# Performance work log

Measured on AMD Instinct MI355X. Metric: run time of the kernel, lower is better.

## Reference

```python
import jax, jax.numpy as jnp
import numpy as np

D_MODEL = 1024
NUM_HEADS = 16
HEAD_DIM = D_MODEL // NUM_HEADS
SCALE = 1.0 / np.sqrt(HEAD_DIM).astype(np.float32)


def setup_inputs() -> dict:
    key = jax.random.key(0)
    k1, k2, k3, k4 = jax.random.split(key, 4)
    B, L = 1, 4096
    s = 0.02
    x = jax.random.normal(k1, (B, L, D_MODEL), dtype=jnp.float32)
    W_qkv = jax.random.normal(k2, (D_MODEL, 3 * D_MODEL), dtype=jnp.float32) * s
    W_o = jax.random.normal(k3, (D_MODEL, D_MODEL), dtype=jnp.float32) * s
    b_o = jax.random.normal(k4, (D_MODEL,), dtype=jnp.float32) * s
    return {"x": x, "W_qkv": W_qkv, "W_o": W_o, "b_o": b_o}


def reference(x, W_qkv, W_o, b_o):
    B, L, D = x.shape
    H, Hd = NUM_HEADS, HEAD_DIM
    qkv = x @ W_qkv                          # [B, L, 3D]
    qkv = qkv.reshape(B, L, 3, H, Hd)
    q = jnp.transpose(qkv[:, :, 0], (0, 2, 1, 3))  # [B, H, L, Hd]
    k = jnp.transpose(qkv[:, :, 1], (0, 2, 1, 3))
    v = jnp.transpose(qkv[:, :, 2], (0, 2, 1, 3))
    scores = jnp.einsum("bhqd,bhkd->bhqk", q, k) * SCALE  # [B, H, L, L]
    attn = jax.nn.softmax(scores, axis=-1)
    out = jnp.einsum("bhqk,bhkd->bhqd", attn, v)          # [B, H, L, Hd]
    out = jnp.transpose(out, (0, 2, 1, 3)).reshape(B, L, D)
    return out @ W_o + b_o
```

## Files before the change

kernel.cpp:

```cpp
#include <hip/hip_runtime.h>
#include <stdint.h>


#define L_SEQ 4096
#define DM 1024
#define NHEAD 16
#define HDIM 64
#define ATT_SCALE 0.125f
#define LOG2E 1.4426950408889634f
#define CSC (ATT_SCALE * LOG2E)

typedef __attribute__((ext_vector_type(8))) __bf16 bf16x8;
typedef __attribute__((ext_vector_type(4))) float f32x4;
typedef __attribute__((ext_vector_type(4))) short short4v;

#define GLL16(g, l) __builtin_amdgcn_global_load_lds( \
    (__attribute__((address_space(1))) void*)(g),     \
    (__attribute__((address_space(3))) void*)(l), 16, 0, 0)

#define MFMA32(a, b, c) __builtin_amdgcn_mfma_f32_16x16x32_bf16((a), (b), (c), 0, 0, 0)

__device__ __forceinline__ short f2bf(float f) {
  uint32_t u = __builtin_bit_cast(uint32_t, f);
  u += 0x7fffu + ((u >> 16) & 1u);
  return (short)(u >> 16);
}

__global__ void cast_bf16_kernel(const float* __restrict__ x, short* __restrict__ y, int n4) {
  int i = blockIdx.x * 256 + threadIdx.x;
  if (i < n4) {
    float4 v = ((const float4*)x)[i];
    short4 o;
    o.x = f2bf(v.x); o.y = f2bf(v.y); o.z = f2bf(v.z); o.w = f2bf(v.w);
    ((short4*)y)[i] = o;
  }
}

__global__ void transpose_cast_kernel(const float* __restrict__ W, short* __restrict__ Wt,
                                      int K, int N) {
  __shared__ __align__(16) short t[64 * 66];
  const int kb = blockIdx.y * 64, nb = blockIdx.x * 64;
  const int tid = threadIdx.x;
#pragma unroll
  for (int i = 0; i < 16; i++) {
    int idx = tid + i * 256;
    int r = idx >> 6, c = idx & 63;
    t[r * 66 + c] = f2bf(W[(size_t)(kb + r) * N + nb + c]);
  }
  __syncthreads();
#pragma unroll
  for (int i = 0; i < 16; i++) {
    int idx = tid + i * 256;
    int r = idx >> 6, c = idx & 63;
    Wt[(size_t)(nb + r) * K + kb + c] = t[c * 66 + r];
  }
}

__global__ __launch_bounds__(256, 2)
void gemm128(const short* __restrict__ A, const short* __restrict__ Bt,
             void* __restrict__ out, short* __restrict__ vtout,
             const float* __restrict__ bias,
             int M, int N, int K, int mode) {
  __shared__ __align__(16) short As[4096];
  __shared__ __align__(16) short Bs[4096];
  const int tid = threadIdx.x;
  const int lane = tid & 63;
  const int wave = tid >> 6;
  const int quad = lane >> 4;
  const int cl = lane & 15;
  const int m0 = blockIdx.x * 128;
  const int n0 = blockIdx.y * 128;
  const int wm = (wave >> 1) * 64;
  const int wn = (wave & 1) * 64;

  f32x4 acc[4][4] = {};

  for (int kb = 0; kb < K; kb += 32) {
    __syncthreads();
#pragma unroll
    for (int i = 0; i < 2; i++) {
      int ci = i * 256 + tid;
      int row = ci & 127, c = ci >> 7;
      GLL16(A + (size_t)(m0 + row) * K + kb + c * 8, As + ci * 8);
      GLL16(Bt + (size_t)(n0 + row) * K + kb + c * 8, Bs + ci * 8);
    }
    __syncthreads();
    bf16x8 af[4], bfr[4];
#pragma unroll
    for (int t = 0; t < 4; t++) {
      af[t]  = *(const bf16x8*)(As + (quad * 128 + wm + t * 16 + cl) * 8);
      bfr[t] = *(const bf16x8*)(Bs + (quad * 128 + wn + t * 16 + cl) * 8);
    }
#pragma unroll
    for (int mt = 0; mt < 4; mt++)
#pragma unroll
      for (int nt = 0; nt < 4; nt++)
        acc[mt][nt] = MFMA32(af[mt], bfr[nt], acc[mt][nt]);
  }

  if (mode == 0) {
    short* qkv = (short*)out;
#pragma unroll
    for (int mt = 0; mt < 4; mt++)
#pragma unroll
      for (int nt = 0; nt < 4; nt++) {
        int col = n0 + wn + nt * 16 + cl;
        int which = col >> 10, hd = col & 63;
        int hidx = (col >> 6) & 15;
        int row0 = m0 + wm + mt * 16 + quad * 4;
        if (which == 2) {
          short4v pk;
#pragma unroll
          for (int r = 0; r < 4; r++) pk[r] = f2bf(acc[mt][nt][r]);
          *(short4v*)(vtout + ((size_t)hidx * HDIM + hd) * L_SEQ + row0) = pk;
        } else {
          float sc = (which == 0) ? CSC : 1.0f;
          size_t base = (((size_t)which * NHEAD + hidx) * L_SEQ) * HDIM + hd;
#pragma unroll
          for (int r = 0; r < 4; r++)
            qkv[base + (size_t)(row0 + r) * HDIM] = f2bf(acc[mt][nt][r] * sc);
        }
      }
  } else {
    float* C = (float*)out;
#pragma unroll
    for (int mt = 0; mt < 4; mt++)
#pragma unroll
      for (int nt = 0; nt < 4; nt++) {
        int col = n0 + wn + nt * 16 + cl;
        float b = bias[col];
#pragma unroll
        for (int r = 0; r < 4; r++) {
          int row = m0 + wm + mt * 16 + quad * 4 + r;
          C[(size_t)row * N + col] = acc[mt][nt][r] + b;
        }
      }
  }
}

__global__ __launch_bounds__(256, 4)
void attn_kernel(const short* __restrict__ qkv, const short* __restrict__ vt,
                 short* __restrict__ aout) {
  __shared__ __align__(16) short Ks[2][4096];
  __shared__ __align__(16) short Vs[2][4096];
  const int tid = threadIdx.x, lane = tid & 63, wave = tid >> 6;
  const int quad = lane >> 4, cl = lane & 15;
  const int bid = blockIdx.x;
  const int h  = ((bid & 7) << 1) | ((bid >> 3) & 1);
  const int qb = bid >> 4;
  const short* Qg = qkv + (size_t)h * L_SEQ * HDIM;
  const short* Kg = qkv + ((size_t)NHEAD + h) * L_SEQ * HDIM;
  const short* Vg = vt + (size_t)h * HDIM * L_SEQ;
  const int keyoff = ((cl >> 2) << 3) | (cl & 3);

  bf16x8 qf[2];
  {
    int qrow = qb * 64 + wave * 16 + cl;
    qf[0] = *(const bf16x8*)(Qg + (size_t)qrow * HDIM + quad * 8);
    qf[1] = *(const bf16x8*)(Qg + (size_t)qrow * HDIM + 32 + quad * 8);
  }
  float l_run = 0.f;
  f32x4 o_acc[4] = {};

#define STAGE(t, buf)                                                   \
  {                                                                     \
    _Pragma("unroll")                                                   \
    for (int i = 0; i < 2; i++) {                                       \
      int ci = i * 256 + tid;                                           \
      int row = ci >> 3;                                                \
      int c = (ci & 7) ^ (row & 7);                                     \
      GLL16(Kg + (size_t)((t) * 64 + row) * HDIM + c * 8, &Ks[buf][ci * 8]); \
      GLL16(Vg + (size_t)row * L_SEQ + (t) * 64 + c * 8, &Vs[buf][ci * 8]);  \
    }                                                                   \
  }

  STAGE(0, 0);
  for (int t = 0; t < L_SEQ / 64; t++) {
    const int cur = t & 1;
    __syncthreads();
    if (t + 1 < L_SEQ / 64) STAGE(t + 1, cur ^ 1);

    f32x4 s[2][2] = {};
#pragma unroll
    for (int kslab = 0; kslab < 2; kslab++)
#pragma unroll
      for (int b = 0; b < 2; b++) {
        int krow = kslab * 32 + keyoff + b * 4;
#pragma unroll
        for (int ks = 0; ks < 2; ks++) {
          int c = (ks * 4 + quad) ^ (krow & 7);
          bf16x8 kf = *(const bf16x8*)(&Ks[cur][(krow * 8 + c) * 8]);
          s[kslab][b] = MFMA32(kf, qf[ks], s[kslab][b]);
        }
      }

    bf16x8 vfr[2][4];
#pragma unroll
    for (int kslab = 0; kslab < 2; kslab++)
#pragma unroll
      for (int G = 0; G < 4; G++) {
        int vrow = G * 16 + cl;
        int c = (kslab * 4 + quad) ^ (vrow & 7);
        vfr[kslab][G] = *(const bf16x8*)(&Vs[cur][(vrow * 8 + c) * 8]);
      }

    bf16x8 pbv[2];
#pragma unroll
    for (int kslab = 0; kslab < 2; kslab++)
#pragma unroll
      for (int b = 0; b < 2; b++)
#pragma unroll
        for (int r = 0; r < 4; r++) {
          float pv = __builtin_amdgcn_exp2f(s[kslab][b][r]);
          l_run += pv;
          pbv[kslab][b * 4 + r] = (__bf16)pv;
        }

#pragma unroll
    for (int kslab = 0; kslab < 2; kslab++)
#pragma unroll
      for (int G = 0; G < 4; G++)
        o_acc[G] = MFMA32(vfr[kslab][G], pbv[kslab], o_acc[G]);
  }
#undef STAGE

  {
    float rs = l_run;
    rs += __shfl_xor(rs, 16);
    rs += __shfl_xor(rs, 32);
    float inv = 1.f / rs;
    int token = qb * 64 + wave * 16 + cl;
#pragma unroll
    for (int G = 0; G < 4; G++) {
      short4v pk;
#pragma unroll
      for (int r = 0; r < 4; r++) pk[r] = f2bf(o_acc[G][r] * inv);
      *(short4v*)(aout + (size_t)token * DM + h * HDIM + G * 16 + quad * 4) = pk;
    }
  }
}

extern "C" void kernel_launch(void* const* d_in, const int* in_sizes, int n_in,
                              void* d_out, int out_size, void* d_ws, size_t ws_size,
                              hipStream_t stream) {
  const float* x    = (const float*)d_in[0];
  const float* Wqkv = (const float*)d_in[1];
  const float* Wo   = (const float*)d_in[2];
  const float* bo   = (const float*)d_in[3];
  char* ws = (char*)d_ws;
  short* xb    = (short*)(ws);
  short* wqkvt = (short*)(ws + (size_t)8 * 1024 * 1024);
  short* wot   = (short*)(ws + (size_t)14 * 1024 * 1024);
  short* qkv   = (short*)(ws + (size_t)16 * 1024 * 1024);
  short* vt    = (short*)(ws + (size_t)40 * 1024 * 1024);
  short* aout  = xb;
  float* out = (float*)d_out;

  cast_bf16_kernel<<<4096, 256, 0, stream>>>(x, xb, L_SEQ * DM / 4);
  transpose_cast_kernel<<<dim3(48, 16), 256, 0, stream>>>(Wqkv, wqkvt, DM, 3 * DM);
  transpose_cast_kernel<<<dim3(16, 16), 256, 0, stream>>>(Wo, wot, DM, DM);
  gemm128<<<dim3(32, 24), 256, 0, stream>>>(xb, wqkvt, qkv, vt, nullptr, L_SEQ, 3 * DM, DM, 0);
  attn_kernel<<<dim3(1024), 256, 0, stream>>>(qkv, vt, aout);
  gemm128<<<dim3(32, 8), 256, 0, stream>>>(aout, wot, out, nullptr, bo, L_SEQ, DM, DM, 1);
}
```

Measured before the change: 260.0 us.

## Fuse prep kernels, retile output GEMM, compute softmax denominator via MFMA

Merges the input cast and both weight transpose-casts into one launch, and splits the GEMM into a QKV variant and a narrower 128x64-tile output GEMM that gives more blocks for the smaller projection. In attention, it precomputes staging pointers, changes the LDS swizzle pattern, and replaces the scalar row-sum with an MFMA against a ones vector. It also uses vector bf16 conversion builtins. The aim is to cut launch overhead and VALU work in the attention loop, and to improve occupancy in the output GEMM, at the cost of an extra MFMA per slab and different rounding behaviour.

```diff
diff --git a/kernel.cpp b/kernel.cpp
--- a/kernel.cpp
+++ b/kernel.cpp
@@ -11,8 +11,11 @@
 #define CSC (ATT_SCALE * LOG2E)
 
 typedef __attribute__((ext_vector_type(8))) __bf16 bf16x8;
+typedef __attribute__((ext_vector_type(4))) __bf16 bf16x4;
 typedef __attribute__((ext_vector_type(4))) float f32x4;
+typedef __attribute__((ext_vector_type(8))) float f32x8;
 typedef __attribute__((ext_vector_type(4))) short short4v;
+typedef __attribute__((ext_vector_type(8))) short short8v;
 
 #define GLL16(g, l) __builtin_amdgcn_global_load_lds( \
     (__attribute__((address_space(1))) void*)(g),     \
@@ -26,41 +29,48 @@
   return (short)(u >> 16);
 }
 
-__global__ void cast_bf16_kernel(const float* __restrict__ x, short* __restrict__ y, int n4) {
-  int i = blockIdx.x * 256 + threadIdx.x;
-  if (i < n4) {
+__global__ __launch_bounds__(256)
+void prep_kernel(const float* __restrict__ x, short* __restrict__ xb,
+                 const float* __restrict__ Wq, short* __restrict__ wqt,
+                 const float* __restrict__ Wo, short* __restrict__ wot) {
+  __shared__ __align__(16) short tbuf[64 * 66];
+  const int tid = threadIdx.x;
+  const int blk = blockIdx.x;
+  if (blk < 4096) {
+    int i = blk * 256 + tid;
     float4 v = ((const float4*)x)[i];
     short4 o;
     o.x = f2bf(v.x); o.y = f2bf(v.y); o.z = f2bf(v.z); o.w = f2bf(v.w);
-    ((short4*)y)[i] = o;
-  }
-}
-
-__global__ void transpose_cast_kernel(const float* __restrict__ W, short* __restrict__ Wt,
-                                      int K, int N) {
-  __shared__ __align__(16) short t[64 * 66];
-  const int kb = blockIdx.y * 64, nb = blockIdx.x * 64;
-  const int tid = threadIdx.x;
+    ((short4*)xb)[i] = o;
+    return;
+  }
+  const float* W; short* Wt; int N, nb, kb;
+  const int K = 1024;
+  if (blk < 4096 + 768) {
+    int b = blk - 4096;
+    W = Wq; Wt = wqt; N = 3072; nb = (b % 48) * 64; kb = (b / 48) * 64;
+  } else {
+    int b = blk - (4096 + 768);
+    W = Wo; Wt = wot; N = 1024; nb = (b % 16) * 64; kb = (b / 16) * 64;
+  }
 #pragma unroll
   for (int i = 0; i < 16; i++) {
     int idx = tid + i * 256;
     int r = idx >> 6, c = idx & 63;
-    t[r * 66 + c] = f2bf(W[(size_t)(kb + r) * N + nb + c]);
+    tbuf[r * 66 + c] = f2bf(W[(size_t)(kb + r) * N + nb + c]);
   }
   __syncthreads();
 #pragma unroll
   for (int i = 0; i < 16; i++) {
     int idx = tid + i * 256;
     int r = idx >> 6, c = idx & 63;
-    Wt[(size_t)(nb + r) * K + kb + c] = t[c * 66 + r];
+    Wt[(size_t)(nb + r) * K + kb + c] = tbuf[c * 66 + r];
   }
 }
 
 __global__ __launch_bounds__(256, 2)
-void gemm128(const short* __restrict__ A, const short* __restrict__ Bt,
-             void* __restrict__ out, short* __restrict__ vtout,
-             const float* __restrict__ bias,
-             int M, int N, int K, int mode) {
+void gemm_qkv(const short* __restrict__ A, const short* __restrict__ Bt,
+              short* __restrict__ qkv, short* __restrict__ vtout, int K) {
   __shared__ __align__(16) short As[4096];
   __shared__ __align__(16) short Bs[4096];
   const int tid = threadIdx.x;
@@ -98,44 +108,82 @@
         acc[mt][nt] = MFMA32(af[mt], bfr[nt], acc[mt][nt]);
   }
 
-  if (mode == 0) {
-    short* qkv = (short*)out;
+#pragma unroll
+  for (int mt = 0; mt < 4; mt++)
+#pragma unroll
+    for (int nt = 0; nt < 4; nt++) {
+      int col = n0 + wn + nt * 16 + cl;
+      int which = col >> 10, hd = col & 63;
+      int hidx = (col >> 6) & 15;
+      int row0 = m0 + wm + mt * 16 + quad * 4;
+      if (which == 2) {
+        short4v pk;
+#pragma unroll
+        for (int r = 0; r < 4; r++) pk[r] = f2bf(acc[mt][nt][r]);
+        *(short4v*)(vtout + ((size_t)hidx * HDIM + hd) * L_SEQ + row0) = pk;
+      } else {
+        float sc = (which == 0) ? CSC : 1.0f;
+        size_t base = (((size_t)which * NHEAD + hidx) * L_SEQ) * HDIM + hd;
+#pragma unroll
+        for (int r = 0; r < 4; r++)
+          qkv[base + (size_t)(row0 + r) * HDIM] = f2bf(acc[mt][nt][r] * sc);
+      }
+    }
+}
+
+__global__ __launch_bounds__(256, 2)
+void gemm_out(const short* __restrict__ A, const short* __restrict__ Bt,
+              float* __restrict__ C, const float* __restrict__ bias, int K) {
+  __shared__ __align__(16) short As[4096];
+  __shared__ __align__(16) short Bs[2048];
+  const int tid = threadIdx.x;
+  const int lane = tid & 63;
+  const int wave = tid >> 6;
+  const int quad = lane >> 4;
+  const int cl = lane & 15;
+  const int m0 = blockIdx.x * 128;
+  const int n0 = blockIdx.y * 64;
+  const int wm = (wave >> 1) * 64;
+  const int wn = (wave & 1) * 32;
+  const int N = 1024;
+
+  f32x4 acc[4][2] = {};
+
+  for (int kb = 0; kb < K; kb += 32) {
+    __syncthreads();
+#pragma unroll
+    for (int i = 0; i < 2; i++) {
+      int ci = i * 256 + tid;
+      GLL16(A + (size_t)(m0 + (ci & 127)) * K + kb + (ci >> 7) * 8, As + ci * 8);
+    }
+    GLL16(Bt + (size_t)(n0 + (tid & 63)) * K + kb + (tid >> 6) * 8, Bs + tid * 8);
+    __syncthreads();
+    bf16x8 af[4], bfr[2];
+#pragma unroll
+    for (int t = 0; t < 4; t++)
+      af[t] = *(const bf16x8*)(As + (quad * 128 + wm + t * 16 + cl) * 8);
+#pragma unroll
+    for (int t = 0; t < 2; t++)
+      bfr[t] = *(const bf16x8*)(Bs + (quad * 64 + wn + t * 16 + cl) * 8);
 #pragma unroll
     for (int mt = 0; mt < 4; mt++)
 #pragma unroll
-      for (int nt = 0; nt < 4; nt++) {
-        int col = n0 + wn + nt * 16 + cl;
-        int which = col >> 10, hd = col & 63;
-        int hidx = (col >> 6) & 15;
-        int row0 = m0 + wm + mt * 16 + quad * 4;
-        if (which == 2) {
-          short4v pk;
-#pragma unroll
-          for (int r = 0; r < 4; r++) pk[r] = f2bf(acc[mt][nt][r]);
-          *(short4v*)(vtout + ((size_t)hidx * HDIM + hd) * L_SEQ + row0) = pk;
-        } else {
-          float sc = (which == 0) ? CSC : 1.0f;
-          size_t base = (((size_t)which * NHEAD + hidx) * L_SEQ) * HDIM + hd;
-#pragma unroll
-          for (int r = 0; r < 4; r++)
-            qkv[base + (size_t)(row0 + r) * HDIM] = f2bf(acc[mt][nt][r] * sc);
-        }
+      for (int nt = 0; nt < 2; nt++)
+        acc[mt][nt] = MFMA32(af[mt], bfr[nt], acc[mt][nt]);
+  }
+
+#pragma unroll
+  for (int mt = 0; mt < 4; mt++)
+#pragma unroll
+    for (int nt = 0; nt < 2; nt++) {
+      int col = n0 + wn + nt * 16 + cl;
+      float b = bias[col];
+#pragma unroll
+      for (int r = 0; r < 4; r++) {
+        int row = m0 + wm + mt * 16 + quad * 4 + r;
+        C[(size_t)row * N + col] = acc[mt][nt][r] + b;
       }
-  } else {
-    float* C = (float*)out;
-#pragma unroll
-    for (int mt = 0; mt < 4; mt++)
-#pragma unroll
-      for (int nt = 0; nt < 4; nt++) {
-        int col = n0 + wn + nt * 16 + cl;
-        float b = bias[col];
-#pragma unroll
-        for (int r = 0; r < 4; r++) {
-          int row = m0 + wm + mt * 16 + quad * 4 + r;
-          C[(size_t)row * N + col] = acc[mt][nt][r] + b;
-        }
-      }
-  }
+    }
 }
 
 __global__ __launch_bounds__(256, 4)
@@ -159,19 +207,29 @@
     qf[0] = *(const bf16x8*)(Qg + (size_t)qrow * HDIM + quad * 8);
     qf[1] = *(const bf16x8*)(Qg + (size_t)qrow * HDIM + 32 + quad * 8);
   }
-  float l_run = 0.f;
+  const short8v ov = {0x3F80, 0x3F80, 0x3F80, 0x3F80, 0x3F80, 0x3F80, 0x3F80, 0x3F80};
+  const bf16x8 ones = __builtin_bit_cast(bf16x8, ov);
+  f32x4 o_l = {};
   f32x4 o_acc[4] = {};
 
-#define STAGE(t, buf)                                                   \
-  {                                                                     \
-    _Pragma("unroll")                                                   \
-    for (int i = 0; i < 2; i++) {                                       \
-      int ci = i * 256 + tid;                                           \
-      int row = ci >> 3;                                                \
-      int c = (ci & 7) ^ (row & 7);                                     \
-      GLL16(Kg + (size_t)((t) * 64 + row) * HDIM + c * 8, &Ks[buf][ci * 8]); \
-      GLL16(Vg + (size_t)row * L_SEQ + (t) * 64 + c * 8, &Vs[buf][ci * 8]);  \
-    }                                                                   \
+  const short* kp[2]; const short* vp[2]; int ldso[2];
+#pragma unroll
+  for (int i = 0; i < 2; i++) {
+    int ci = i * 256 + tid;
+    int row = ci >> 3;
+    int sw = (row & 3) | (((row >> 3) & 1) << 2);
+    int c = (ci & 7) ^ sw;
+    kp[i] = Kg + (size_t)row * HDIM + c * 8;
+    vp[i] = Vg + (size_t)row * L_SEQ + c * 8;
+    ldso[i] = ci * 8;
+  }
+#define STAGE(t, buf)                                       \
+  {                                                         \
+    _Pragma("unroll")                                       \
+    for (int i = 0; i < 2; i++) {                           \
+      GLL16(kp[i] + (t) * 64 * HDIM, &Ks[buf][ldso[i]]);    \
+      GLL16(vp[i] + (t) * 64, &Vs[buf][ldso[i]]);           \
+    }                                                       \
   }
 
   STAGE(0, 0);
@@ -186,9 +244,10 @@
 #pragma unroll
       for (int b = 0; b < 2; b++) {
         int krow = kslab * 32 + keyoff + b * 4;
+        int sw = (krow & 3) | (((krow >> 3) & 1) << 2);
 #pragma unroll
         for (int ks = 0; ks < 2; ks++) {
-          int c = (ks * 4 + quad) ^ (krow & 7);
+          int c = (ks * 4 + quad) ^ sw;
           bf16x8 kf = *(const bf16x8*)(&Ks[cur][(krow * 8 + c) * 8]);
           s[kslab][b] = MFMA32(kf, qf[ks], s[kslab][b]);
         }
@@ -200,21 +259,23 @@
 #pragma unroll
       for (int G = 0; G < 4; G++) {
         int vrow = G * 16 + cl;
-        int c = (kslab * 4 + quad) ^ (vrow & 7);
+        int sw = (vrow & 3) | (((vrow >> 3) & 1) << 2);
+        int c = (kslab * 4 + quad) ^ sw;
         vfr[kslab][G] = *(const bf16x8*)(&Vs[cur][(vrow * 8 + c) * 8]);
       }
 
     bf16x8 pbv[2];
 #pragma unroll
-    for (int kslab = 0; kslab < 2; kslab++)
+    for (int kslab = 0; kslab < 2; kslab++) {
+      f32x8 pv8;
 #pragma unroll
       for (int b = 0; b < 2; b++)
 #pragma unroll
-        for (int r = 0; r < 4; r++) {
-          float pv = __builtin_amdgcn_exp2f(s[kslab][b][r]);
-          l_run += pv;
-          pbv[kslab][b * 4 + r] = (__bf16)pv;
-        }
+        for (int r = 0; r < 4; r++)
+          pv8[b * 4 + r] = __builtin_amdgcn_exp2f(s[kslab][b][r]);
+      pbv[kslab] = __builtin_convertvector(pv8, bf16x8);
+      o_l = MFMA32(ones, pbv[kslab], o_l);
+    }
 
 #pragma unroll
     for (int kslab = 0; kslab < 2; kslab++)
@@ -225,17 +286,14 @@
 #undef STAGE
 
   {
-    float rs = l_run;
-    rs += __shfl_xor(rs, 16);
-    rs += __shfl_xor(rs, 32);
-    float inv = 1.f / rs;
+    float inv = 1.f / o_l[0];
     int token = qb * 64 + wave * 16 + cl;
 #pragma unroll
     for (int G = 0; G < 4; G++) {
-      short4v pk;
-#pragma unroll
-      for (int r = 0; r < 4; r++) pk[r] = f2bf(o_acc[G][r] * inv);
-      *(short4v*)(aout + (size_t)token * DM + h * HDIM + G * 16 + quad * 4) = pk;
+      f32x4 sc = o_acc[G] * inv;
+      bf16x4 pk = __builtin_convertvector(sc, bf16x4);
+      *(short4v*)(aout + (size_t)token * DM + h * HDIM + G * 16 + quad * 4) =
+          __builtin_bit_cast(short4v, pk);
     }
   }
 }
@@ -256,10 +314,8 @@
   short* aout  = xb;
   float* out = (float*)d_out;
 
-  cast_bf16_kernel<<<4096, 256, 0, stream>>>(x, xb, L_SEQ * DM / 4);
-  transpose_cast_kernel<<<dim3(48, 16), 256, 0, stream>>>(Wqkv, wqkvt, DM, 3 * DM);
-  transpose_cast_kernel<<<dim3(16, 16), 256, 0, stream>>>(Wo, wot, DM, DM);
-  gemm128<<<dim3(32, 24), 256, 0, stream>>>(xb, wqkvt, qkv, vt, nullptr, L_SEQ, 3 * DM, DM, 0);
+  prep_kernel<<<4096 + 768 + 256, 256, 0, stream>>>(x, xb, Wqkv, wqkvt, Wo, wot);
+  gemm_qkv<<<dim3(32, 24), 256, 0, stream>>>(xb, wqkvt, qkv, vt, DM);
   attn_kernel<<<dim3(1024), 256, 0, stream>>>(qkv, vt, aout);
-  gemm128<<<dim3(32, 8), 256, 0, stream>>>(aout, wot, out, nullptr, bo, L_SEQ, DM, DM, 1);
-}
+  gemm_out<<<dim3(32, 16), 256, 0, stream>>>(aout, wot, out, bo, DM);
+}
```

After: 247.9 us. 4.6% less time.
